# Kernel tuning notes

Hardware: AMD Instinct MI355X
Metric: run time of the kernel (lower is better)

The kernel has to match this reference:

```python
import jax, jax.numpy as jnp
import numpy as np

N_NODES = 20000; N_EDGES = 200000
FN = 128; FE = 64; D = 128; T = 128; K = 5
H = 4; DH = D // H; N_LAYERS = 2; FF = 4 * D
B = 32768
T0 = 0.0; EPS = 1e-5


def _ln(x, s, b):
    m = jnp.mean(x, axis=-1, keepdims=True)
    v = jnp.mean(jnp.square(x - m), axis=-1, keepdims=True)
    return (x - m) / jnp.sqrt(v + EPS) * s + b


def setup_inputs() -> dict:
    key = jax.random.key(0)
    ks = jax.random.split(key, 24)
    def w(i, shape, s=0.05):
        return jax.random.normal(ks[i], shape, jnp.float32) * s
    return {
        "src": jax.random.randint(ks[0], (B,), 0, N_NODES),
        "dst": jax.random.randint(ks[1], (B,), 0, N_NODES),
        "neg": jax.random.randint(ks[2], (B,), 0, N_NODES),
        "eidx": jax.random.randint(ks[3], (B,), 0, N_EDGES),
        "ts": jax.random.uniform(ks[4], (B,), jnp.float32) * 1000.0,
        "node_feats": w(5, (N_NODES, FN), 1.0),
        "edge_feats": w(6, (N_EDGES, FE), 1.0),
        "node_lin_w": w(7, (D, FN)), "node_lin_b": jnp.zeros((D,), jnp.float32),
        "edge_lin_w": w(8, (D, FE)), "edge_lin_b": jnp.zeros((D,), jnp.float32),
        "time_w": w(9, (T,), 1.0), "time_b": w(10, (T,), 1.0),
        "tok_w": w(11, (D, 3 * D + T)), "tok_b": jnp.zeros((D,), jnp.float32),
        "qkv_w": w(12, (N_LAYERS, 3 * D, D)), "qkv_b": jnp.zeros((N_LAYERS, 3 * D), jnp.float32),
        "attn_w": w(13, (N_LAYERS, D, D)), "attn_b": jnp.zeros((N_LAYERS, D), jnp.float32),
        "ln1_s": jnp.ones((N_LAYERS, D), jnp.float32), "ln1_b": jnp.zeros((N_LAYERS, D), jnp.float32),
        "ln2_s": jnp.ones((N_LAYERS, D), jnp.float32), "ln2_b": jnp.zeros((N_LAYERS, D), jnp.float32),
        "ff1_w": w(14, (N_LAYERS, FF, D)), "ff1_b": jnp.zeros((N_LAYERS, FF), jnp.float32),
        "ff2_w": w(15, (N_LAYERS, D, FF)), "ff2_b": jnp.zeros((N_LAYERS, D), jnp.float32),
        "p1_w": w(16, (D, D)), "p1_b": jnp.zeros((D,), jnp.float32),
        "p2_w": w(17, (K, D)), "p2_b": jnp.zeros((K,), jnp.float32),
    }


def reference(src, dst, neg, eidx, ts, node_feats, edge_feats,
              node_lin_w, node_lin_b, edge_lin_w, edge_lin_b,
              time_w, time_b, tok_w, tok_b,
              qkv_w, qkv_b, attn_w, attn_b,
              ln1_s, ln1_b, ln2_s, ln2_b,
              ff1_w, ff1_b, ff2_w, ff2_b,
              p1_w, p1_b, p2_w, p2_b):
    # --- occurrence tokens: [src occs | dst occs | neg occs] = 3B tokens ---
    self_nodes = jnp.concatenate([src, dst, neg])          # [3B]
    other_nodes = jnp.concatenate([dst, src, src])         # [3B]
    eidx_all = jnp.concatenate([eidx, eidx, eidx])
    ts_all = jnp.concatenate([ts, ts, ts])
    Ntot = self_nodes.shape[0]

    base_self = node_feats[self_nodes] @ node_lin_w.T + node_lin_b    # [3B, D]
    base_other = node_feats[other_nodes] @ node_lin_w.T + node_lin_b
    edge_emb = edge_feats[eidx_all] @ edge_lin_w.T + edge_lin_b       # [3B, D]
    time_emb = jnp.cos((ts_all - T0)[:, None] * time_w[None, :] + time_b)  # [3B, T]
    x_cat = jnp.concatenate([base_self, base_other, edge_emb, time_emb], axis=-1)
    tok = jax.nn.relu(x_cat @ tok_w.T + tok_b)                        # [3B, D]

    # --- group occurrences by node, sort by time, pad (device-side) ---
    node_ids = jnp.unique(self_nodes)                      # [Nn]
    order = jnp.lexsort((ts_all, self_nodes))              # primary node, secondary time
    nodes_s = self_nodes[order]
    row_s = jnp.searchsorted(node_ids, nodes_s)            # row per sorted occ
    starts = jnp.searchsorted(nodes_s, node_ids)           # start of each group
    pos_s = jnp.arange(Ntot) - starts[row_s]               # pos within group
    node_row = jnp.zeros((Ntot,), jnp.int32).at[order].set(row_s.astype(jnp.int32))
    pos_map = jnp.zeros((Ntot,), jnp.int32).at[order].set(pos_s.astype(jnp.int32))
    seq_len = jnp.diff(jnp.concatenate([starts, jnp.array([Ntot], starts.dtype)]))
    Nn = int(node_ids.shape[0])
    Lmax = int(seq_len.max())

    x_pad = jnp.zeros((Nn, Lmax, D), tok.dtype).at[node_row, pos_map].set(tok)
    pad_mask = jnp.arange(Lmax)[None, :] >= seq_len[:, None]  # True = padded key

    # --- pre-LN TransformerEncoder (gelu, no final norm) ---
    scale = jnp.float32(1.0 / np.sqrt(DH))
    x = x_pad
    for l in range(N_LAYERS):
        h = _ln(x, ln1_s[l], ln1_b[l])
        qkv = h @ qkv_w[l].T + qkv_b[l]                    # [Nn, L, 3D]
        q, k, v = jnp.split(qkv, 3, axis=-1)
        q = q.reshape(Nn, Lmax, H, DH); k = k.reshape(Nn, Lmax, H, DH); v = v.reshape(Nn, Lmax, H, DH)
        scores = jnp.einsum('nqhd,nkhd->nhqk', q, k) * scale
        scores = jnp.where(pad_mask[:, None, None, :], jnp.float32(-1e9), scores)
        a = jax.nn.softmax(scores, axis=-1)
        o = jnp.einsum('nhqk,nkhd->nqhd', a, v).reshape(Nn, Lmax, D)
        x = x + o @ attn_w[l].T + attn_b[l]
        h2 = _ln(x, ln2_s[l], ln2_b[l])
        x = x + jax.nn.gelu(h2 @ ff1_w[l].T + ff1_b[l], approximate=False) @ ff2_w[l].T + ff2_b[l]

    # --- gather per-occurrence outputs and project to community probs ---
    def proj(hh):
        return jax.nn.softmax(jax.nn.relu(hh @ p1_w.T + p1_b) @ p2_w.T + p2_b, axis=-1)
    src_h = x[node_row[:B], pos_map[:B]]
    dst_h = x[node_row[B:2 * B], pos_map[B:2 * B]]
    neg_h = x[node_row[2 * B:], pos_map[2 * B:]]
    return proj(src_h), proj(dst_h), proj(neg_h)
```

## Files before the change

### kernel.cpp

```cpp
#include <hip/hip_runtime.h>
#include <hip/hip_bf16.h>
#include <math.h>

#define NB 32768
#define NTOK (3 * NB)
#define NNODES 20000
#define MAXL 64

typedef short bf16x8 __attribute__((ext_vector_type(8)));
typedef float f32x4 __attribute__((ext_vector_type(4)));

typedef __attribute__((address_space(3))) void lds_t;
typedef const __attribute__((address_space(1))) void gbl_t;

__device__ __forceinline__ float b2f(short s) {
    unsigned int u = ((unsigned int)(unsigned short)s) << 16;
    union { unsigned int u; float f; } c;
    c.u = u;
    return c.f;
}


__global__ void convert_k(const float* __restrict__ in, __hip_bfloat16* __restrict__ out, int n) {
    int i = blockIdx.x * 256 + threadIdx.x;
    int stride = gridDim.x * 256;
    for (; i < n; i += stride) out[i] = __float2bfloat16(in[i]);
}

__global__ void fold12_k(const float* __restrict__ tok_w, const float* __restrict__ nl_w,
                         __hip_bfloat16* __restrict__ A12) {
    int idx = blockIdx.x * 256 + threadIdx.x;
    if (idx >= 256 * 128) return;
    int n = idx >> 7, f = idx & 127;
    const float* tw = (n < 128) ? (tok_w + n * 512) : (tok_w + (n - 128) * 512 + 128);
    float acc = 0.f;
    for (int c = 0; c < 128; ++c) acc += tw[c] * nl_w[c * 128 + f];
    A12[idx] = __float2bfloat16(acc);
}

__global__ void foldE_k(const float* __restrict__ tok_w, const float* __restrict__ el_w,
                        __hip_bfloat16* __restrict__ AE) {
    int idx = blockIdx.x * 256 + threadIdx.x;
    if (idx >= 128 * 192) return;
    int d = idx / 192, j = idx % 192;
    float acc;
    if (j < 64) {
        acc = 0.f;
        for (int c = 0; c < 128; ++c) acc += tok_w[d * 512 + 256 + c] * el_w[c * 64 + j];
    } else {
        acc = tok_w[d * 512 + 384 + (j - 64)];
    }
    AE[idx] = __float2bfloat16(acc);
}

__global__ void foldb_k(const float* __restrict__ tok_w, const float* __restrict__ tok_b,
                        const float* __restrict__ nl_b, const float* __restrict__ el_b,
                        float* __restrict__ bf) {
    int d = threadIdx.x;
    if (d >= 128) return;
    float acc = tok_b[d];
    for (int c = 0; c < 128; ++c)
        acc += (tok_w[d * 512 + c] + tok_w[d * 512 + 128 + c]) * nl_b[c];
    for (int c = 0; c < 128; ++c)
        acc += tok_w[d * 512 + 256 + c] * el_b[c];
    bf[d] = acc;
}

__device__ __forceinline__ int self_node(int t, const int* src, const int* dst, const int* neg) {
    if (t < NB) return src[t];
    if (t < 2 * NB) return dst[t - NB];
    return neg[t - 2 * NB];
}

__global__ void count_k(const int* __restrict__ src, const int* __restrict__ dst,
                        const int* __restrict__ neg, int* __restrict__ cnt) {
    int t = blockIdx.x * 256 + threadIdx.x;
    if (t >= NTOK) return;
    atomicAdd(&cnt[self_node(t, src, dst, neg)], 1);
}

__global__ __launch_bounds__(1024) void scan_k(const int* __restrict__ cnt,
                                               int* __restrict__ starts) {
    __shared__ int ps[1024];
    int t = threadIdx.x;
    const int PER = 20;
    int base = t * PER;
    int loc[PER];
    int s = 0;
#pragma unroll
    for (int k = 0; k < PER; ++k) {
        int i = base + k;
        int v = (i < NNODES) ? cnt[i] : 0;
        loc[k] = s;
        s += v;
    }
    ps[t] = s;
    __syncthreads();
    for (int off = 1; off < 1024; off <<= 1) {
        int v = (t >= off) ? ps[t - off] : 0;
        __syncthreads();
        ps[t] += v;
        __syncthreads();
    }
    int offv = (t > 0) ? ps[t - 1] : 0;
#pragma unroll
    for (int k = 0; k < PER; ++k) {
        int i = base + k;
        if (i < NNODES) starts[i] = offv + loc[k];
    }
}

__global__ void scatter_k(const int* __restrict__ src, const int* __restrict__ dst,
                          const int* __restrict__ neg, const int* __restrict__ starts,
                          int* __restrict__ cursor, int* __restrict__ order) {
    int t = blockIdx.x * 256 + threadIdx.x;
    if (t >= NTOK) return;
    int node = self_node(t, src, dst, neg);
    int p = atomicAdd(&cursor[node], 1);
    order[starts[node] + p] = t;
}

__global__ void aemb_k(const int* __restrict__ eidx, const float* __restrict__ ts,
                       const float* __restrict__ ef, const float* __restrict__ tw,
                       const float* __restrict__ tb, __hip_bfloat16* __restrict__ Aemb) {
    int idx = blockIdx.x * 256 + threadIdx.x;
    if (idx >= NB * 192) return;
    int m = idx / 192, j = idx % 192;
    float v;
    if (j < 64) v = ef[(size_t)eidx[m] * 64 + j];
    else { int c = j - 64; v = cosf(ts[m] * tw[c] + tb[c]); }
    Aemb[idx] = __float2bfloat16(v);
}

__global__ __launch_bounds__(256) void asm_emb_k(
    const int* __restrict__ order, const int* __restrict__ src, const int* __restrict__ dst,
    const int* __restrict__ neg, const float* __restrict__ P12, const float* __restrict__ E,
    const float* __restrict__ s, const float* __restrict__ b,
    float* __restrict__ x, __hip_bfloat16* __restrict__ h) {
    int p = blockIdx.x * 4 + (threadIdx.x >> 6);
    int lane = threadIdx.x & 63;
    int t = order[p];
    int m, self, other;
    if (t < NB) { m = t; self = src[m]; other = dst[m]; }
    else if (t < 2 * NB) { m = t - NB; self = dst[m]; other = src[m]; }
    else { m = t - 2 * NB; self = neg[m]; other = src[m]; }
    int d0 = lane, d1 = lane + 64;
    float v0 = P12[(size_t)self * 256 + d0] + P12[(size_t)other * 256 + 128 + d0] +
               E[(size_t)m * 128 + d0];
    float v1 = P12[(size_t)self * 256 + d1] + P12[(size_t)other * 256 + 128 + d1] +
               E[(size_t)m * 128 + d1];
    v0 = fmaxf(v0, 0.f);
    v1 = fmaxf(v1, 0.f);
    float sum = v0 + v1;
#pragma unroll
    for (int off = 32; off; off >>= 1) sum += __shfl_xor(sum, off, 64);
    float mean = sum * (1.f / 128.f);
    float c0 = v0 - mean, c1 = v1 - mean;
    float vs = c0 * c0 + c1 * c1;
#pragma unroll
    for (int off = 32; off; off >>= 1) vs += __shfl_xor(vs, off, 64);
    float inv = rsqrtf(vs * (1.f / 128.f) + 1e-5f);
    x[(size_t)p * 128 + d0] = v0;
    x[(size_t)p * 128 + d1] = v1;
    h[(size_t)p * 128 + d0] = __float2bfloat16(c0 * inv * s[d0] + b[d0]);
    h[(size_t)p * 128 + d1] = __float2bfloat16(c1 * inv * s[d1] + b[d1]);
}

__device__ __forceinline__ float gelu_f(float v) {
    float ax = fabsf(v) * 0.70710678118654752f;
    float t = 1.f / (1.f + 0.3275911f * ax);
    float poly = ((((1.061405429f * t - 1.453152027f) * t + 1.421413741f) * t -
                   0.284496736f) * t + 0.254829592f) * t;
    float erf_ax = 1.f - poly * __expf(-ax * ax);
    float erfv = (v < 0.f) ? -erf_ax : erf_ax;
    return 0.5f * v * (1.f + erfv);
}

#define G_F32 0
#define G_BF16 1
#define G_GELU 2
#define G_ADD_LN 3
#define G_ADD_BF16 4

template <int MODE>
__global__ __launch_bounds__(256, 3) void gemm5_k(
    const __hip_bfloat16* __restrict__ A, const __hip_bfloat16* __restrict__ B,
    const float* __restrict__ bias, float* __restrict__ x,
    const float* __restrict__ lns, const float* __restrict__ lnb,
    __hip_bfloat16* __restrict__ hout, float* __restrict__ Cf, int N, int K) {
    __shared__ __align__(16) __hip_bfloat16 sA[3 * 128 * 32];
    __shared__ __align__(16) __hip_bfloat16 sB[3 * 128 * 32];
    __shared__ float redS[2][128];
    __shared__ float redS2[2][128];
    int tid = threadIdx.x;
    int lane = tid & 63, wid = tid >> 6;
    int wm = wid & 1, wn = wid >> 1;
    int mBase = blockIdx.x * 128, nBase = blockIdx.y * 128;
    f32x4 acc[4][4];
#pragma unroll
    for (int i = 0; i < 4; ++i)
#pragma unroll
        for (int j = 0; j < 4; ++j) {
            f32x4 z = {0.f, 0.f, 0.f, 0.f};
            acc[i][j] = z;
        }

    auto stage = [&](int buf, int k0) {
#pragma unroll
        for (int i = 0; i < 2; ++i) {
            int cid = i * 256 + tid;
            int row = cid >> 2, slotS = cid & 3;
            int slotG = slotS ^ ((row & 3) ^ ((row >> 2) & 3));
            const __hip_bfloat16* ga = A + (size_t)(mBase + row) * K + k0 + slotG * 8;
            const __hip_bfloat16* gb = B + (size_t)(nBase + row) * K + k0 + slotG * 8;
            __builtin_amdgcn_global_load_lds(
                (gbl_t*)ga, (lds_t*)&sA[buf * 4096 + (cid & ~63) * 8], 16, 0, 0);
            __builtin_amdgcn_global_load_lds(
                (gbl_t*)gb, (lds_t*)&sB[buf * 4096 + (cid & ~63) * 8], 16, 0, 0);
        }
    };

    int nt = K >> 5;
    stage(0, 0);
    int cur = 0;
    for (int t = 0; t < nt; ++t) {
        int nxt = cur + 1;
        if (nxt == 3) nxt = 0;
        if (t + 1 < nt) {
            stage(nxt, (t + 1) << 5);
            asm volatile("s_waitcnt vmcnt(4)" ::: "memory");
        } else {
            asm volatile("s_waitcnt vmcnt(0)" ::: "memory");
        }
        __builtin_amdgcn_s_barrier();
        __builtin_amdgcn_sched_barrier(0);
        const bf16x8* AsV = reinterpret_cast<const bf16x8*>(sA + cur * 4096);
        const bf16x8* BsV = reinterpret_cast<const bf16x8*>(sB + cur * 4096);
        bf16x8 a[4], b[4];
        int kvec = lane >> 4;
#pragma unroll
        for (int f = 0; f < 4; ++f) {
            int ra = wm * 64 + f * 16 + (lane & 15);
            a[f] = AsV[ra * 4 + (kvec ^ ((ra & 3) ^ ((ra >> 2) & 3)))];
            int rb = wn * 64 + f * 16 + (lane & 15);
            b[f] = BsV[rb * 4 + (kvec ^ ((rb & 3) ^ ((rb >> 2) & 3)))];
        }
        __builtin_amdgcn_s_setprio(1);
#pragma unroll
        for (int fm = 0; fm < 4; ++fm)
#pragma unroll
            for (int fn = 0; fn < 4; ++fn)
                acc[fm][fn] = __builtin_amdgcn_mfma_f32_16x16x32_bf16(
                    a[fm], b[fn], acc[fm][fn], 0, 0, 0);
        __builtin_amdgcn_s_setprio(0);
        cur = nxt;
    }

    if (MODE == G_F32 || MODE == G_BF16 || MODE == G_GELU) {
        int colBase = nBase + wn * 64;
#pragma unroll
        for (int fm = 0; fm < 4; ++fm) {
            int row0 = mBase + wm * 64 + fm * 16 + (lane >> 4) * 4;
#pragma unroll
            for (int fn = 0; fn < 4; ++fn) {
                int col = colBase + fn * 16 + (lane & 15);
                float bv = bias ? bias[col] : 0.f;
#pragma unroll
                for (int j = 0; j < 4; ++j) {
                    float v = acc[fm][fn][j] + bv;
                    if (MODE == G_F32) {
                        Cf[(size_t)(row0 + j) * N + col] = v;
                    } else if (MODE == G_GELU) {
                        hout[(size_t)(row0 + j) * N + col] = __float2bfloat16(gelu_f(v));
                    } else {
                        hout[(size_t)(row0 + j) * N + col] = __float2bfloat16(v);
                    }
                }
            }
        }
    } else {
#pragma unroll
        for (int fm = 0; fm < 4; ++fm) {
            int rl0 = wm * 64 + fm * 16 + (lane >> 4) * 4;
#pragma unroll
            for (int fn = 0; fn < 4; ++fn) {
                int col = wn * 64 + fn * 16 + (lane & 15);
                float bv = bias[col];
#pragma unroll
                for (int j = 0; j < 4; ++j) {
                    size_t off = (size_t)(mBase + rl0 + j) * 128 + col;
                    float v = acc[fm][fn][j] + bv + x[off];
                    x[off] = v;
                    acc[fm][fn][j] = v;
                }
            }
        }
        if (MODE == G_ADD_BF16) {
#pragma unroll
            for (int fm = 0; fm < 4; ++fm) {
                int rl0 = wm * 64 + fm * 16 + (lane >> 4) * 4;
#pragma unroll
                for (int fn = 0; fn < 4; ++fn) {
                    int col = wn * 64 + fn * 16 + (lane & 15);
#pragma unroll
                    for (int j = 0; j < 4; ++j)
                        hout[(size_t)(mBase + rl0 + j) * 128 + col] =
                            __float2bfloat16(acc[fm][fn][j]);
                }
            }
        } else {
#pragma unroll
            for (int fm = 0; fm < 4; ++fm) {
#pragma unroll
                for (int j = 0; j < 4; ++j) {
                    float s1 = 0.f, s2 = 0.f;
#pragma unroll
                    for (int fn = 0; fn < 4; ++fn) {
                        float v = acc[fm][fn][j];
                        s1 += v;
                        s2 += v * v;
                    }
#pragma unroll
                    for (int off = 1; off < 16; off <<= 1) {
                        s1 += __shfl_xor(s1, off, 64);
                        s2 += __shfl_xor(s2, off, 64);
                    }
                    if ((lane & 15) == 0) {
                        int rl = wm * 64 + fm * 16 + (lane >> 4) * 4 + j;
                        redS[wn][rl] = s1;
                        redS2[wn][rl] = s2;
                    }
                }
            }
            __syncthreads();
#pragma unroll
            for (int fm = 0; fm < 4; ++fm) {
                int rl0 = wm * 64 + fm * 16 + (lane >> 4) * 4;
#pragma unroll
                for (int j = 0; j < 4; ++j) {
                    int rl = rl0 + j;
                    float mean = (redS[0][rl] + redS[1][rl]) * (1.f / 128.f);
                    float var = (redS2[0][rl] + redS2[1][rl]) * (1.f / 128.f) - mean * mean;
                    float inv = rsqrtf(var + 1e-5f);
#pragma unroll
                    for (int fn = 0; fn < 4; ++fn) {
                        int col = wn * 64 + fn * 16 + (lane & 15);
                        float c = (acc[fm][fn][j] - mean) * inv;
                        hout[(size_t)(mBase + rl) * 128 + col] =
                            __float2bfloat16(c * lns[col] + lnb[col]);
                    }
                }
            }
        }
    }
}

__global__ __launch_bounds__(256) void attn_k(
    const __hip_bfloat16* __restrict__ qkv, const int* __restrict__ starts,
    const int* __restrict__ cnt, __hip_bfloat16* __restrict__ o) {
    __shared__ float sc[4][4][4][MAXL];
    int wid = threadIdx.x >> 6, lane = threadIdx.x & 63;
    int node = blockIdx.x * 4 + wid;
    if (node >= NNODES) return;
    int st = starts[node];
    int len = cnt[node];
    if (len <= 0) return;
    if (len > MAXL) len = MAXL;
    int qs = lane >> 4, li = lane & 15, h = li >> 2;
    const float scale = 0.17677669529663687f;

    for (int qb = 0; qb < len; qb += 4) {
        int qi = qb + qs;
        bool act = qi < len;
        int qidx = act ? qi : len - 1;
        bf16x8 qv = *reinterpret_cast<const bf16x8*>(
            qkv + (size_t)(st + qidx) * 384 + li * 8);
        float qf[8];
#pragma unroll
        for (int e = 0; e < 8; ++e) qf[e] = b2f(qv[e]);
        for (int j = 0; j < len; ++j) {
            bf16x8 kv = *reinterpret_cast<const bf16x8*>(
                qkv + (size_t)(st + j) * 384 + 128 + li * 8);
            float d = 0.f;
#pragma unroll
            for (int e = 0; e < 8; ++e) d += qf[e] * b2f(kv[e]);
            d += __shfl_xor(d, 1, 64);
            d += __shfl_xor(d, 2, 64);
            if ((li & 3) == 0) sc[wid][qs][h][j] = d * scale;
        }
        float mx = -1e30f;
        for (int j = li & 3; j < len; j += 4) mx = fmaxf(mx, sc[wid][qs][h][j]);
        mx = fmaxf(mx, __shfl_xor(mx, 1, 64));
        mx = fmaxf(mx, __shfl_xor(mx, 2, 64));
        float ssum = 0.f;
        for (int j = li & 3; j < len; j += 4) {
            float e = __expf(sc[wid][qs][h][j] - mx);
            sc[wid][qs][h][j] = e;
            ssum += e;
        }
        ssum += __shfl_xor(ssum, 1, 64);
        ssum += __shfl_xor(ssum, 2, 64);
        float sinv = 1.f / ssum;
        float accv[8] = {0.f, 0.f, 0.f, 0.f, 0.f, 0.f, 0.f, 0.f};
        for (int j = 0; j < len; ++j) {
            float p = sc[wid][qs][h][j];
            bf16x8 vv = *reinterpret_cast<const bf16x8*>(
                qkv + (size_t)(st + j) * 384 + 256 + li * 8);
#pragma unroll
            for (int e = 0; e < 8; ++e) accv[e] += p * b2f(vv[e]);
        }
        if (act) {
            bf16x8 ov;
#pragma unroll
            for (int e = 0; e < 8; ++e) {
                __hip_bfloat16 t = __float2bfloat16(accv[e] * sinv);
                ov[e] = *reinterpret_cast<short*>(&t);
            }
            *reinterpret_cast<bf16x8*>(o + (size_t)(st + qi) * 128 + li * 8) = ov;
        }
    }
}

__global__ __launch_bounds__(256) void p1head_k(
    const __hip_bfloat16* __restrict__ A, const __hip_bfloat16* __restrict__ B,
    const float* __restrict__ bias, const float* __restrict__ p2w,
    const float* __restrict__ p2b, const int* __restrict__ order,
    float* __restrict__ out) {
    __shared__ __align__(16) char smem[65536];
    __shared__ float p2s[640];
    __shared__ float p2bs[5];
    float4* As4 = (float4*)smem;
    float4* Bs4 = (float4*)(smem + 16384);
    float* rowbuf = (float*)smem;
    int tid = threadIdx.x;
    for (int i = tid; i < 640; i += 256) p2s[i] = p2w[i];
    if (tid < 5) p2bs[tid] = p2b[tid];
    int lane = tid & 63, wid = tid >> 6;
    int wm = wid & 1, wn = wid >> 1;
    int mBase = blockIdx.x * 128;
    f32x4 acc[4][4];
#pragma unroll
    for (int i = 0; i < 4; ++i)
#pragma unroll
        for (int j = 0; j < 4; ++j) {
            f32x4 z = {0.f, 0.f, 0.f, 0.f};
            acc[i][j] = z;
        }
    bf16x8* AsV = reinterpret_cast<bf16x8*>(As4);
    bf16x8* BsV = reinterpret_cast<bf16x8*>(Bs4);
    for (int k0 = 0; k0 < 128; k0 += 64) {
#pragma unroll
        for (int i = 0; i < 4; ++i) {
            int cid = i * 256 + tid;
            int r = cid >> 3, c = cid & 7;
            int sidx = r * 8 + (c ^ (r & 7));
            As4[sidx] = *reinterpret_cast<const float4*>(A + (size_t)(mBase + r) * 128 + k0 + c * 8);
            Bs4[sidx] = *reinterpret_cast<const float4*>(B + (size_t)r * 128 + k0 + c * 8);
        }
        __syncthreads();
#pragma unroll
        for (int kk = 0; kk < 2; ++kk) {
            bf16x8 a[4], bb[4];
            int ccol = kk * 4 + (lane >> 4);
#pragma unroll
            for (int f = 0; f < 4; ++f) {
                int ra = wm * 64 + f * 16 + (lane & 15);
                a[f] = AsV[ra * 8 + (ccol ^ (ra & 7))];
                int rb = wn * 64 + f * 16 + (lane & 15);
                bb[f] = BsV[rb * 8 + (ccol ^ (rb & 7))];
            }
#pragma unroll
            for (int fm = 0; fm < 4; ++fm)
#pragma unroll
                for (int fn = 0; fn < 4; ++fn)
                    acc[fm][fn] = __builtin_amdgcn_mfma_f32_16x16x32_bf16(
                        a[fm], bb[fn], acc[fm][fn], 0, 0, 0);
        }
        __syncthreads();
    }
#pragma unroll
    for (int fm = 0; fm < 4; ++fm) {
        int rl0 = wm * 64 + fm * 16 + (lane >> 4) * 4;
#pragma unroll
        for (int fn = 0; fn < 4; ++fn) {
            int col = wn * 64 + fn * 16 + (lane & 15);
            float bv = bias[col];
#pragma unroll
            for (int j = 0; j < 4; ++j) {
                int rl = rl0 + j;
                rowbuf[rl * 128 + (col ^ ((rl & 7) << 2))] = fmaxf(acc[fm][fn][j] + bv, 0.f);
            }
        }
    }
    __syncthreads();
    int row = tid >> 1, half = tid & 1;
    int swz = (row & 7) << 2;
    float lg[5] = {0.f, 0.f, 0.f, 0.f, 0.f};
    for (int i = 0; i < 64; ++i) {
        int col = half * 64 + i;
        float rv = rowbuf[row * 128 + (col ^ swz)];
#pragma unroll
        for (int k = 0; k < 5; ++k) lg[k] += rv * p2s[k * 128 + col];
    }
#pragma unroll
    for (int k = 0; k < 5; ++k) lg[k] += __shfl_xor(lg[k], 1, 64);
    if (half == 0) {
        float mx = -1e30f;
#pragma unroll
        for (int k = 0; k < 5; ++k) {
            lg[k] += p2bs[k];
            mx = fmaxf(mx, lg[k]);
        }
        float e[5], ssum = 0.f;
#pragma unroll
        for (int k = 0; k < 5; ++k) {
            e[k] = __expf(lg[k] - mx);
            ssum += e[k];
        }
        float si = 1.f / ssum;
        int t = order[mBase + row];
#pragma unroll
        for (int k = 0; k < 5; ++k) out[(size_t)t * 5 + k] = e[k] * si;
    }
}


extern "C" void kernel_launch(void* const* d_in, const int* in_sizes, int n_in,
                              void* d_out, int out_size, void* d_ws, size_t ws_size,
                              hipStream_t stream) {
    const int* src = (const int*)d_in[0];
    const int* dst = (const int*)d_in[1];
    const int* neg = (const int*)d_in[2];
    const int* eidx = (const int*)d_in[3];
    const float* ts = (const float*)d_in[4];
    const float* node_feats = (const float*)d_in[5];
    const float* edge_feats = (const float*)d_in[6];
    const float* node_lin_w = (const float*)d_in[7];
    const float* node_lin_b = (const float*)d_in[8];
    const float* edge_lin_w = (const float*)d_in[9];
    const float* edge_lin_b = (const float*)d_in[10];
    const float* time_w = (const float*)d_in[11];
    const float* time_b = (const float*)d_in[12];
    const float* tok_w = (const float*)d_in[13];
    const float* tok_b = (const float*)d_in[14];
    const float* qkv_w = (const float*)d_in[15];
    const float* qkv_b = (const float*)d_in[16];
    const float* attn_w = (const float*)d_in[17];
    const float* attn_b = (const float*)d_in[18];
    const float* ln1_s = (const float*)d_in[19];
    const float* ln1_b = (const float*)d_in[20];
    const float* ln2_s = (const float*)d_in[21];
    const float* ln2_b = (const float*)d_in[22];
    const float* ff1_w = (const float*)d_in[23];
    const float* ff1_b = (const float*)d_in[24];
    const float* ff2_w = (const float*)d_in[25];
    const float* ff2_b = (const float*)d_in[26];
    const float* p1_w = (const float*)d_in[27];
    const float* p1_b = (const float*)d_in[28];
    const float* p2_w = (const float*)d_in[29];
    const float* p2_b = (const float*)d_in[30];
    float* out = (float*)d_out;

    char* w = (char*)d_ws;
    auto alloc = [&](size_t bytes) {
        char* p = w;
        w += (bytes + 255) & ~(size_t)255;
        return p;
    };
    float* x = (float*)alloc((size_t)NTOK * 128 * 4);
    __hip_bfloat16* h = (__hip_bfloat16*)alloc((size_t)NTOK * 128 * 2);
    char* big = alloc((size_t)(NTOK + 64) * 512 * 2);
    __hip_bfloat16* qkvb = (__hip_bfloat16*)big;
    __hip_bfloat16* ob = (__hip_bfloat16*)(big + (size_t)(NTOK + 64) * 384 * 2);
    __hip_bfloat16* ub = (__hip_bfloat16*)big;
    float* P12 = (float*)alloc((size_t)(NNODES + 96) * 256 * 4);
    float* E = (float*)alloc((size_t)NB * 128 * 4);
    __hip_bfloat16* Aemb = (__hip_bfloat16*)alloc((size_t)NB * 192 * 2);
    __hip_bfloat16* nfb = (__hip_bfloat16*)alloc((size_t)(NNODES + 96) * 128 * 2);
    __hip_bfloat16* A12 = (__hip_bfloat16*)alloc(256 * 128 * 2);
    __hip_bfloat16* AE = (__hip_bfloat16*)alloc(128 * 192 * 2);
    float* bfold = (float*)alloc(128 * 4);
    __hip_bfloat16* qkvwb = (__hip_bfloat16*)alloc(2 * 384 * 128 * 2);
    __hip_bfloat16* attnwb = (__hip_bfloat16*)alloc(2 * 128 * 128 * 2);
    __hip_bfloat16* ff1wb = (__hip_bfloat16*)alloc(2 * 512 * 128 * 2);
    __hip_bfloat16* ff2wb = (__hip_bfloat16*)alloc(2 * 128 * 512 * 2);
    __hip_bfloat16* p1wb = (__hip_bfloat16*)alloc(128 * 128 * 2);
    int* cnt = (int*)alloc(NNODES * 4);
    int* starts = (int*)alloc(NNODES * 4);
    int* cursor = (int*)alloc(NNODES * 4);
    int* order = (int*)alloc(NTOK * 4);

    hipMemsetAsync(cnt, 0, NNODES * 4, stream);
    hipMemsetAsync(cursor, 0, NNODES * 4, stream);

    auto cvt = [&](const float* in, __hip_bfloat16* outp, int n) {
        int blocks = (n + 255) / 256;
        if (blocks > 2048) blocks = 2048;
        convert_k<<<blocks, 256, 0, stream>>>(in, outp, n);
    };
    cvt(node_feats, nfb, NNODES * 128);
    cvt(qkv_w, qkvwb, 2 * 384 * 128);
    cvt(attn_w, attnwb, 2 * 128 * 128);
    cvt(ff1_w, ff1wb, 2 * 512 * 128);
    cvt(ff2_w, ff2wb, 2 * 128 * 512);
    cvt(p1_w, p1wb, 128 * 128);

    fold12_k<<<128, 256, 0, stream>>>(tok_w, node_lin_w, A12);
    foldE_k<<<96, 256, 0, stream>>>(tok_w, edge_lin_w, AE);
    foldb_k<<<1, 128, 0, stream>>>(tok_w, tok_b, node_lin_b, edge_lin_b, bfold);

    count_k<<<(NTOK + 255) / 256, 256, 0, stream>>>(src, dst, neg, cnt);
    scan_k<<<1, 1024, 0, stream>>>(cnt, starts);
    scatter_k<<<(NTOK + 255) / 256, 256, 0, stream>>>(src, dst, neg, starts, cursor, order);

    aemb_k<<<(NB * 192 + 255) / 256, 256, 0, stream>>>(eidx, ts, edge_feats, time_w, time_b, Aemb);

    gemm5_k<G_F32><<<dim3(157, 2), 256, 0, stream>>>(
        nfb, A12, nullptr, nullptr, nullptr, nullptr, nullptr, P12, 256, 128);
    gemm5_k<G_F32><<<dim3(256, 1), 256, 0, stream>>>(
        Aemb, AE, bfold, nullptr, nullptr, nullptr, nullptr, E, 128, 192);
    asm_emb_k<<<NTOK / 4, 256, 0, stream>>>(order, src, dst, neg, P12, E,
                                            ln1_s, ln1_b, x, h);

    const int gm = NTOK / 128;

    for (int l = 0; l < 2; ++l) {
        gemm5_k<G_BF16><<<dim3(gm, 3), 256, 0, stream>>>(
            h, qkvwb + (size_t)l * 384 * 128, qkv_b + l * 384,
            nullptr, nullptr, nullptr, qkvb, nullptr, 384, 128);
        attn_k<<<(NNODES + 3) / 4, 256, 0, stream>>>(qkvb, starts, cnt, ob);
        gemm5_k<G_ADD_LN><<<dim3(gm, 1), 256, 0, stream>>>(
            ob, attnwb + (size_t)l * 128 * 128, attn_b + l * 128,
            x, ln2_s + l * 128, ln2_b + l * 128, h, nullptr, 128, 128);
        gemm5_k<G_GELU><<<dim3(gm, 4), 256, 0, stream>>>(
            h, ff1wb + (size_t)l * 512 * 128, ff1_b + l * 512,
            nullptr, nullptr, nullptr, ub, nullptr, 512, 128);
        if (l == 0)
            gemm5_k<G_ADD_LN><<<dim3(gm, 1), 256, 0, stream>>>(
                ub, ff2wb, ff2_b, x, ln1_s + 128, ln1_b + 128, h, nullptr, 128, 512);
        else
            gemm5_k<G_ADD_BF16><<<dim3(gm, 1), 256, 0, stream>>>(
                ub, ff2wb + (size_t)128 * 512, ff2_b + 128, x,
                nullptr, nullptr, h, nullptr, 128, 512);
    }

    p1head_k<<<gm, 256, 0, stream>>>(h, p1wb, p1_b, p2_w, p2_b, order, out);
}
```

Measured before the change: 573.1 us.

## Fuse FFN up-projection, GELU and down-projection into one kernel

Replaces the separate FF1 (GELU) and FF2 (add+LN) GEMM launches with a single ffn_k kernel. It keeps the 512-wide intermediate in registers, chunked by 64 columns, and feeds it straight into the second MFMA. The FF2 weight is pre-permuted at conversion time so the GELU accumulator layout lines up with the MFMA operand layout. This removes the round trip of the large bf16 intermediate through global memory, in exchange for lower occupancy (launch bounds 2) and more register pressure per block.

```diff
diff --git a/kernel.cpp b/kernel.cpp
--- a/kernel.cpp
+++ b/kernel.cpp
@@ -25,6 +25,15 @@
     int i = blockIdx.x * 256 + threadIdx.x;
     int stride = gridDim.x * 256;
     for (; i < n; i += stride) out[i] = __float2bfloat16(in[i]);
+}
+
+__global__ void cvtw2_k(const float* __restrict__ in, __hip_bfloat16* __restrict__ out) {
+    int idx = blockIdx.x * 256 + threadIdx.x;
+    if (idx >= 2 * 128 * 512) return;
+    int row = idx >> 9, kk = idx & 511;
+    int s = kk >> 5, p = kk & 31;
+    int src = (s << 5) + ((p >> 2) & 1) * 16 + ((p >> 3) << 2) + (p & 3);
+    out[idx] = __float2bfloat16(in[(size_t)row * 512 + src]);
 }
 
 __global__ void fold12_k(const float* __restrict__ tok_w, const float* __restrict__ nl_w,
@@ -178,9 +187,7 @@
 
 #define G_F32 0
 #define G_BF16 1
-#define G_GELU 2
 #define G_ADD_LN 3
-#define G_ADD_BF16 4
 
 template <int MODE>
 __global__ __launch_bounds__(256, 3) void gemm5_k(
@@ -256,7 +263,7 @@
         cur = nxt;
     }
 
-    if (MODE == G_F32 || MODE == G_BF16 || MODE == G_GELU) {
+    if (MODE == G_F32 || MODE == G_BF16) {
         int colBase = nBase + wn * 64;
 #pragma unroll
         for (int fm = 0; fm < 4; ++fm) {
@@ -268,13 +275,8 @@
 #pragma unroll
                 for (int j = 0; j < 4; ++j) {
                     float v = acc[fm][fn][j] + bv;
-                    if (MODE == G_F32) {
-                        Cf[(size_t)(row0 + j) * N + col] = v;
-                    } else if (MODE == G_GELU) {
-                        hout[(size_t)(row0 + j) * N + col] = __float2bfloat16(gelu_f(v));
-                    } else {
-                        hout[(size_t)(row0 + j) * N + col] = __float2bfloat16(v);
-                    }
+                    if (MODE == G_F32) Cf[(size_t)(row0 + j) * N + col] = v;
+                    else hout[(size_t)(row0 + j) * N + col] = __float2bfloat16(v);
                 }
             }
         }
@@ -295,60 +297,204 @@
                 }
             }
         }
-        if (MODE == G_ADD_BF16) {
-#pragma unroll
-            for (int fm = 0; fm < 4; ++fm) {
-                int rl0 = wm * 64 + fm * 16 + (lane >> 4) * 4;
+#pragma unroll
+        for (int fm = 0; fm < 4; ++fm) {
+#pragma unroll
+            for (int j = 0; j < 4; ++j) {
+                float s1 = 0.f, s2 = 0.f;
+#pragma unroll
+                for (int fn = 0; fn < 4; ++fn) {
+                    float v = acc[fm][fn][j];
+                    s1 += v;
+                    s2 += v * v;
+                }
+#pragma unroll
+                for (int off = 1; off < 16; off <<= 1) {
+                    s1 += __shfl_xor(s1, off, 64);
+                    s2 += __shfl_xor(s2, off, 64);
+                }
+                if ((lane & 15) == 0) {
+                    int rl = wm * 64 + fm * 16 + (lane >> 4) * 4 + j;
+                    redS[wn][rl] = s1;
+                    redS2[wn][rl] = s2;
+                }
+            }
+        }
+        __syncthreads();
+#pragma unroll
+        for (int fm = 0; fm < 4; ++fm) {
+            int rl0 = wm * 64 + fm * 16 + (lane >> 4) * 4;
+#pragma unroll
+            for (int j = 0; j < 4; ++j) {
+                int rl = rl0 + j;
+                float mean = (redS[0][rl] + redS[1][rl]) * (1.f / 128.f);
+                float var = (redS2[0][rl] + redS2[1][rl]) * (1.f / 128.f) - mean * mean;
+                float inv = rsqrtf(var + 1e-5f);
 #pragma unroll
                 for (int fn = 0; fn < 4; ++fn) {
                     int col = wn * 64 + fn * 16 + (lane & 15);
-#pragma unroll
-                    for (int j = 0; j < 4; ++j)
-                        hout[(size_t)(mBase + rl0 + j) * 128 + col] =
-                            __float2bfloat16(acc[fm][fn][j]);
-                }
-            }
+                    float c = (acc[fm][fn][j] - mean) * inv;
+                    hout[(size_t)(mBase + rl) * 128 + col] =
+                        __float2bfloat16(c * lns[col] + lnb[col]);
+                }
+            }
+        }
+    }
+}
+
+template <bool DO_LN>
+__global__ __launch_bounds__(256, 2) void ffn_k(
+    const __hip_bfloat16* __restrict__ h, const __hip_bfloat16* __restrict__ W1,
+    const float* __restrict__ b1, const __hip_bfloat16* __restrict__ W2p,
+    const float* __restrict__ b2, float* __restrict__ x,
+    const float* __restrict__ lns, const float* __restrict__ lnb,
+    __hip_bfloat16* __restrict__ hout) {
+    __shared__ __align__(16) __hip_bfloat16 w1s[2][64 * 128];
+    __shared__ __align__(16) __hip_bfloat16 w2s[2][128 * 64];
+    __shared__ float b1s[512];
+    int tid = threadIdx.x;
+    int lane = tid & 63, wid = tid >> 6;
+    int li = lane & 15, q = lane >> 4;
+    int mBase = blockIdx.x * 128;
+
+    b1s[tid] = b1[tid];
+    b1s[256 + tid] = b1[256 + tid];
+
+    bf16x8 hf[2][4];
+#pragma unroll
+    for (int t = 0; t < 2; ++t)
+#pragma unroll
+        for (int kk = 0; kk < 4; ++kk)
+            hf[t][kk] = *reinterpret_cast<const bf16x8*>(
+                h + (size_t)(mBase + wid * 32 + t * 16 + li) * 128 + (kk * 4 + q) * 8);
+
+    auto stageW = [&](int buf, int c) {
+#pragma unroll
+        for (int i = 0; i < 4; ++i) {
+            int cid = i * 256 + tid;
+            int r1 = cid >> 4, s1 = cid & 15;
+            int g1 = s1 ^ (r1 & 15);
+            __builtin_amdgcn_global_load_lds(
+                (gbl_t*)(W1 + (size_t)(c * 64 + r1) * 128 + g1 * 8),
+                (lds_t*)&w1s[buf][(cid & ~63) * 8], 16, 0, 0);
+            int r2 = cid >> 3, s2 = cid & 7;
+            int g2 = s2 ^ (r2 & 7);
+            __builtin_amdgcn_global_load_lds(
+                (gbl_t*)(W2p + (size_t)r2 * 512 + c * 64 + g2 * 8),
+                (lds_t*)&w2s[buf][(cid & ~63) * 8], 16, 0, 0);
+        }
+    };
+
+    f32x4 acc2[2][8];
+#pragma unroll
+    for (int t = 0; t < 2; ++t)
+#pragma unroll
+        for (int o = 0; o < 8; ++o) {
+            f32x4 z = {0.f, 0.f, 0.f, 0.f};
+            acc2[t][o] = z;
+        }
+
+    stageW(0, 0);
+    for (int c = 0; c < 8; ++c) {
+        if (c + 1 < 8) {
+            stageW((c + 1) & 1, c + 1);
+            asm volatile("s_waitcnt vmcnt(8) lgkmcnt(0)" ::: "memory");
         } else {
-#pragma unroll
-            for (int fm = 0; fm < 4; ++fm) {
-#pragma unroll
-                for (int j = 0; j < 4; ++j) {
-                    float s1 = 0.f, s2 = 0.f;
-#pragma unroll
-                    for (int fn = 0; fn < 4; ++fn) {
-                        float v = acc[fm][fn][j];
-                        s1 += v;
-                        s2 += v * v;
-                    }
-#pragma unroll
-                    for (int off = 1; off < 16; off <<= 1) {
-                        s1 += __shfl_xor(s1, off, 64);
-                        s2 += __shfl_xor(s2, off, 64);
-                    }
-                    if ((lane & 15) == 0) {
-                        int rl = wm * 64 + fm * 16 + (lane >> 4) * 4 + j;
-                        redS[wn][rl] = s1;
-                        redS2[wn][rl] = s2;
-                    }
-                }
-            }
-            __syncthreads();
-#pragma unroll
-            for (int fm = 0; fm < 4; ++fm) {
-                int rl0 = wm * 64 + fm * 16 + (lane >> 4) * 4;
-#pragma unroll
-                for (int j = 0; j < 4; ++j) {
-                    int rl = rl0 + j;
-                    float mean = (redS[0][rl] + redS[1][rl]) * (1.f / 128.f);
-                    float var = (redS2[0][rl] + redS2[1][rl]) * (1.f / 128.f) - mean * mean;
-                    float inv = rsqrtf(var + 1e-5f);
-#pragma unroll
-                    for (int fn = 0; fn < 4; ++fn) {
-                        int col = wn * 64 + fn * 16 + (lane & 15);
-                        float c = (acc[fm][fn][j] - mean) * inv;
-                        hout[(size_t)(mBase + rl) * 128 + col] =
-                            __float2bfloat16(c * lns[col] + lnb[col]);
-                    }
+            asm volatile("s_waitcnt vmcnt(0) lgkmcnt(0)" ::: "memory");
+        }
+        __builtin_amdgcn_s_barrier();
+        __builtin_amdgcn_sched_barrier(0);
+        const bf16x8* W1v = reinterpret_cast<const bf16x8*>(w1s[c & 1]);
+        const bf16x8* W2v = reinterpret_cast<const bf16x8*>(w2s[c & 1]);
+        f32x4 acc1[4][2];
+#pragma unroll
+        for (int f = 0; f < 4; ++f)
+#pragma unroll
+            for (int t = 0; t < 2; ++t) {
+                f32x4 z = {0.f, 0.f, 0.f, 0.f};
+                acc1[f][t] = z;
+            }
+#pragma unroll
+        for (int kk = 0; kk < 4; ++kk) {
+            bf16x8 a[4];
+#pragma unroll
+            for (int f = 0; f < 4; ++f) {
+                int r = f * 16 + li;
+                a[f] = W1v[r * 16 + ((kk * 4 + q) ^ (r & 15))];
+            }
+            __builtin_amdgcn_s_setprio(1);
+#pragma unroll
+            for (int f = 0; f < 4; ++f)
+#pragma unroll
+                for (int t = 0; t < 2; ++t)
+                    acc1[f][t] = __builtin_amdgcn_mfma_f32_16x16x32_bf16(
+                        a[f], hf[t][kk], acc1[f][t], 0, 0, 0);
+            __builtin_amdgcn_s_setprio(0);
+        }
+#pragma unroll
+        for (int s = 0; s < 2; ++s) {
+            bf16x8 uf[2];
+#pragma unroll
+            for (int t = 0; t < 2; ++t) {
+#pragma unroll
+                for (int e = 0; e < 8; ++e) {
+                    int f = 2 * s + (e >> 2);
+                    float v = acc1[f][t][e & 3] + b1s[c * 64 + f * 16 + q * 4 + (e & 3)];
+                    v = gelu_f(v);
+                    __hip_bfloat16 bb = __float2bfloat16(v);
+                    uf[t][e] = *reinterpret_cast<short*>(&bb);
+                }
+            }
+#pragma unroll
+            for (int o = 0; o < 8; ++o) {
+                int rb = o * 16 + li;
+                bf16x8 w2f = W2v[rb * 8 + ((s * 4 + q) ^ (rb & 7))];
+#pragma unroll
+                for (int t = 0; t < 2; ++t)
+                    acc2[t][o] = __builtin_amdgcn_mfma_f32_16x16x32_bf16(
+                        uf[t], w2f, acc2[t][o], 0, 0, 0);
+            }
+        }
+        __builtin_amdgcn_s_barrier();
+    }
+
+#pragma unroll
+    for (int t = 0; t < 2; ++t) {
+#pragma unroll
+        for (int j = 0; j < 4; ++j) {
+            int row = mBase + wid * 32 + t * 16 + q * 4 + j;
+            float s1 = 0.f, s2 = 0.f;
+#pragma unroll
+            for (int o = 0; o < 8; ++o) {
+                int col = o * 16 + li;
+                size_t off = (size_t)row * 128 + col;
+                float v = acc2[t][o][j] + b2[col] + x[off];
+                if (DO_LN) x[off] = v;
+                acc2[t][o][j] = v;
+                s1 += v;
+                s2 += v * v;
+            }
+#pragma unroll
+            for (int off2 = 1; off2 < 16; off2 <<= 1) {
+                s1 += __shfl_xor(s1, off2, 64);
+                s2 += __shfl_xor(s2, off2, 64);
+            }
+            if (DO_LN) {
+                float mean = s1 * (1.f / 128.f);
+                float var = s2 * (1.f / 128.f) - mean * mean;
+                float inv = rsqrtf(var + 1e-5f);
+#pragma unroll
+                for (int o = 0; o < 8; ++o) {
+                    int col = o * 16 + li;
+                    float cc = (acc2[t][o][j] - mean) * inv;
+                    hout[(size_t)row * 128 + col] =
+                        __float2bfloat16(cc * lns[col] + lnb[col]);
+                }
+            } else {
+#pragma unroll
+                for (int o = 0; o < 8; ++o) {
+                    int col = o * 16 + li;
+                    hout[(size_t)row * 128 + col] = __float2bfloat16(acc2[t][o][j]);
                 }
             }
         }
@@ -572,7 +718,6 @@
     char* big = alloc((size_t)(NTOK + 64) * 512 * 2);
     __hip_bfloat16* qkvb = (__hip_bfloat16*)big;
     __hip_bfloat16* ob = (__hip_bfloat16*)(big + (size_t)(NTOK + 64) * 384 * 2);
-    __hip_bfloat16* ub = (__hip_bfloat16*)big;
     float* P12 = (float*)alloc((size_t)(NNODES + 96) * 256 * 4);
     float* E = (float*)alloc((size_t)NB * 128 * 4);
     __hip_bfloat16* Aemb = (__hip_bfloat16*)alloc((size_t)NB * 192 * 2);
@@ -583,7 +728,7 @@
     __hip_bfloat16* qkvwb = (__hip_bfloat16*)alloc(2 * 384 * 128 * 2);
     __hip_bfloat16* attnwb = (__hip_bfloat16*)alloc(2 * 128 * 128 * 2);
     __hip_bfloat16* ff1wb = (__hip_bfloat16*)alloc(2 * 512 * 128 * 2);
-    __hip_bfloat16* ff2wb = (__hip_bfloat16*)alloc(2 * 128 * 512 * 2);
+    __hip_bfloat16* w2pb = (__hip_bfloat16*)alloc(2 * 128 * 512 * 2);
     __hip_bfloat16* p1wb = (__hip_bfloat16*)alloc(128 * 128 * 2);
     int* cnt = (int*)alloc(NNODES * 4);
     int* starts = (int*)alloc(NNODES * 4);
@@ -602,7 +747,7 @@
     cvt(qkv_w, qkvwb, 2 * 384 * 128);
     cvt(attn_w, attnwb, 2 * 128 * 128);
     cvt(ff1_w, ff1wb, 2 * 512 * 128);
-    cvt(ff2_w, ff2wb, 2 * 128 * 512);
+    cvtw2_k<<<(2 * 128 * 512 + 255) / 256, 256, 0, stream>>>(ff2_w, w2pb);
     cvt(p1_w, p1wb, 128 * 128);
 
     fold12_k<<<128, 256, 0, stream>>>(tok_w, node_lin_w, A12);
@@ -632,16 +777,13 @@
         gemm5_k<G_ADD_LN><<<dim3(gm, 1), 256, 0, stream>>>(
             ob, attnwb + (size_t)l * 128 * 128, attn_b + l * 128,
             x, ln2_s + l * 128, ln2_b + l * 128, h, nullptr, 128, 128);
-        gemm5_k<G_GELU><<<dim3(gm, 4), 256, 0, stream>>>(
-            h, ff1wb + (size_t)l * 512 * 128, ff1_b + l * 512,
-            nullptr, nullptr, nullptr, ub, nullptr, 512, 128);
         if (l == 0)
-            gemm5_k<G_ADD_LN><<<dim3(gm, 1), 256, 0, stream>>>(
-                ub, ff2wb, ff2_b, x, ln1_s + 128, ln1_b + 128, h, nullptr, 128, 512);
+            ffn_k<true><<<gm, 256, 0, stream>>>(
+                h, ff1wb, ff1_b, w2pb, ff2_b, x, ln1_s + 128, ln1_b + 128, h);
         else
-            gemm5_k<G_ADD_BF16><<<dim3(gm, 1), 256, 0, stream>>>(
-                ub, ff2wb + (size_t)128 * 512, ff2_b + 128, x,
-                nullptr, nullptr, h, nullptr, 128, 512);
+            ffn_k<false><<<gm, 256, 0, stream>>>(
+                h, ff1wb + (size_t)512 * 128, ff1_b + 512, w2pb + (size_t)128 * 512,
+                ff2_b + 128, x, nullptr, nullptr, h);
     }
 
     p1head_k<<<gm, 256, 0, stream>>>(h, p1wb, p1_b, p2_w, p2_b, order, out);
```

New measurement: 512.8 us (median of 2 runs). -10.5%, faster.
